# Performance work log

Measured on AMD Instinct MI355X. Metric: run time of the kernel, lower is better.

Reference implementation:

```python
import jax, jax.numpy as jnp
import numpy as np

N_ATOMS = 50000
N_EDGES = 100000
ATOM_DIM = 64
BOND_DIM = 16


def setup_inputs() -> dict:
    key = jax.random.key(0)
    k1, k2, k3, k4 = jax.random.split(key, 4)
    atom_features = jax.random.normal(k1, (N_ATOMS, ATOM_DIM), dtype=jnp.float32)
    bond_features = jax.random.normal(k2, (N_EDGES, BOND_DIM), dtype=jnp.float32)
    pair_indices = jax.random.randint(k3, (N_EDGES, 2), 0, N_ATOMS, dtype=jnp.int32)
    kernel = jax.random.normal(k4, (BOND_DIM, ATOM_DIM * ATOM_DIM), dtype=jnp.float32) * (1.0 / np.sqrt(BOND_DIM))
    bias = jnp.zeros((ATOM_DIM * ATOM_DIM,), dtype=jnp.float32)
    return {"atom_features": atom_features, "bond_features": bond_features,
            "pair_indices": pair_indices, "kernel": kernel, "bias": bias}


def reference(atom_features, bond_features, pair_indices, kernel, bias):
    n_atoms, d = atom_features.shape
    # per-edge learned linear transform: [E, bond_dim] @ [bond_dim, d*d] -> [E, d, d]
    edge_mats = (bond_features @ kernel + bias).reshape(-1, d, d)
    # gather neighbor atom features (axis 0)
    neighbors = atom_features[pair_indices[:, 1]]  # [E, d]
    # batched matvec: [E, d, d] x [E, d] -> [E, d]
    transformed = jnp.einsum('eij,ej->ei', edge_mats, neighbors)
    # scatter-add to source atoms (true segment_sum, no one-hot materialization)
    aggregated = jax.ops.segment_sum(transformed, pair_indices[:, 0], num_segments=n_atoms)
    return aggregated
```

## Files before the change

### kernel.cpp

```cpp
#include <hip/hip_runtime.h>
#include <hip/hip_bf16.h>


#define N_EDGES   100000
#define DIM       64
#define BDIM      16
#define NB_CH     17
#define KSTEPS    68
#define TILE      32
#define NTILES    (N_EDGES / TILE)
#define GROUPS    4
#define BLOCK     512
#define GRID      256

#define W_BYTES      (KSTEPS * 2 * 64 * 16)
#define NBQ_BYTES    (TILE * DIM * 2)
#define BOND_STRIDE  20
#define BOND_BYTES   (TILE * BOND_STRIDE * 2)
#define SRC_BYTES    (TILE * 4)
#define GROUP_BYTES  (NBQ_BYTES + BOND_BYTES + SRC_BYTES)
#define LDS_TOTAL    (W_BYTES + GROUPS * GROUP_BYTES)

typedef __bf16 bf16x8 __attribute__((ext_vector_type(8)));
typedef float  f32x16 __attribute__((ext_vector_type(16)));

__global__ __launch_bounds__(BLOCK, 2)
void edge_mfma_kernel(const float* __restrict__ atom,
                      const float* __restrict__ bondf,
                      const int*   __restrict__ pair,
                      const float* __restrict__ kmat,
                      const float* __restrict__ bias,
                      float* __restrict__ out)
{
    extern __shared__ char smem[];
    const int tid = threadIdx.x;

    for (int it = 0; it < (KSTEPS * 2 * 64) / BLOCK; ++it) {
        int f   = it * BLOCK + tid;
        int fb  = f >> 6;
        int l   = f & 63;
        int s   = fb >> 1, h = fb & 1;
        int kk0 = s * 16 + ((l >> 5) << 3);
        int n   = h * 32 + (l & 31);
        int b   = kk0 >> 6;
        int jj0 = kk0 & 63;
        const float* src = (b < BDIM) ? (kmat + b * (DIM * DIM) + n * DIM + jj0)
                                      : (bias + n * DIM + jj0);
        float4 v0 = *(const float4*)(src);
        float4 v1 = *(const float4*)(src + 4);
        bf16x8 w;
        w[0] = (__bf16)v0.x; w[1] = (__bf16)v0.y; w[2] = (__bf16)v0.z; w[3] = (__bf16)v0.w;
        w[4] = (__bf16)v1.x; w[5] = (__bf16)v1.y; w[6] = (__bf16)v1.z; w[7] = (__bf16)v1.w;
        *(bf16x8*)(smem + f * 16) = w;
    }
    __syncthreads();

    const int g   = tid >> 7;
    const int tg  = tid & 127;
    const int l   = tid & 63;
    const int wid = tid >> 6;
    const int h   = wid & 1;
    const int ma  = l & 31;
    const int hi  = l >> 5;

    char*   gbase = smem + W_BYTES + g * GROUP_BYTES;
    char*   nbb   = gbase;
    __bf16* bnd   = (__bf16*)(gbase + NBQ_BYTES);
    int*    srcs  = (int*)(gbase + NBQ_BYTES + BOND_BYTES);

    for (int base = blockIdx.x * GROUPS; base < NTILES; base += gridDim.x * GROUPS) {
        int  tile  = base + g;
        bool valid = tile < NTILES;

        if (valid) {
            int m = tg >> 2, p = tg & 3;
            int e = tile * TILE + m;
            int dst = pair[2 * e + 1];
            const float4* ap = (const float4*)(atom + dst * DIM + p * 16);
            float4 a0 = ap[0], a1 = ap[1], a2 = ap[2], a3 = ap[3];
            bf16x8 q0, q1;
            q0[0] = (__bf16)a0.x; q0[1] = (__bf16)a0.y; q0[2] = (__bf16)a0.z; q0[3] = (__bf16)a0.w;
            q0[4] = (__bf16)a1.x; q0[5] = (__bf16)a1.y; q0[6] = (__bf16)a1.z; q0[7] = (__bf16)a1.w;
            q1[0] = (__bf16)a2.x; q1[1] = (__bf16)a2.y; q1[2] = (__bf16)a2.z; q1[3] = (__bf16)a2.w;
            q1[4] = (__bf16)a3.x; q1[5] = (__bf16)a3.y; q1[6] = (__bf16)a3.z; q1[7] = (__bf16)a3.w;
            int sw = m & 7;
            *(bf16x8*)(nbb + m * 128 + (((2 * p    ) ^ sw) << 4)) = q0;
            *(bf16x8*)(nbb + m * 128 + (((2 * p + 1) ^ sw) << 4)) = q1;
            if (p == 0) srcs[m] = pair[2 * e];
            if (tg < TILE) {
                int m2 = tg;
                int e2 = tile * TILE + m2;
                const float4* bp = (const float4*)(bondf + e2 * BDIM);
                float4 b0 = bp[0], b1 = bp[1], b2 = bp[2], b3 = bp[3];
                __bf16* br = bnd + m2 * BOND_STRIDE;
                br[0]  = (__bf16)b0.x; br[1]  = (__bf16)b0.y; br[2]  = (__bf16)b0.z; br[3]  = (__bf16)b0.w;
                br[4]  = (__bf16)b1.x; br[5]  = (__bf16)b1.y; br[6]  = (__bf16)b1.z; br[7]  = (__bf16)b1.w;
                br[8]  = (__bf16)b2.x; br[9]  = (__bf16)b2.y; br[10] = (__bf16)b2.z; br[11] = (__bf16)b2.w;
                br[12] = (__bf16)b3.x; br[13] = (__bf16)b3.y; br[14] = (__bf16)b3.z; br[15] = (__bf16)b3.w;
                br[16] = (__bf16)1.0f;
            }
        }
        __syncthreads();

        if (valid) {
            f32x16 acc;
            #pragma unroll
            for (int i = 0; i < 16; ++i) acc[i] = 0.0f;

            const char*   nbrow = nbb + ma * 128;
            const int     sw    = ma & 7;
            const __bf16* brow  = bnd + ma * BOND_STRIDE;
            const char*   wbase = smem + (h * 64 + l) * 16;

            for (int b = 0; b < NB_CH; ++b) {
                float bv = (float)brow[b];
                #pragma unroll
                for (int ss = 0; ss < 4; ++ss) {
                    bf16x8 nv = *(const bf16x8*)(nbrow + (((ss * 2 + hi) ^ sw) << 4));
                    bf16x8 a;
                    #pragma unroll
                    for (int j = 0; j < 8; ++j)
                        a[j] = (__bf16)(bv * (float)nv[j]);
                    bf16x8 w = *(const bf16x8*)(wbase + (b * 4 + ss) * 2048);
                    acc = __builtin_amdgcn_mfma_f32_32x32x16_bf16(a, w, acc, 0, 0, 0);
                }
            }

            int n = h * 32 + (l & 31);
            #pragma unroll
            for (int r = 0; r < 16; ++r) {
                int m = (r & 3) + 8 * (r >> 2) + 4 * hi;
                atomicAdd(out + srcs[m] * DIM + n, acc[r]);
            }
        }
        __syncthreads();
    }
}

extern "C" void kernel_launch(void* const* d_in, const int* in_sizes, int n_in,
                              void* d_out, int out_size, void* d_ws, size_t ws_size,
                              hipStream_t stream)
{
    const float* atom  = (const float*)d_in[0];
    const float* bondf = (const float*)d_in[1];
    const int*   pair  = (const int*)  d_in[2];
    const float* kmat  = (const float*)d_in[3];
    const float* bias  = (const float*)d_in[4];
    float* out = (float*)d_out;

    hipFuncSetAttribute((const void*)edge_mfma_kernel,
                        hipFuncAttributeMaxDynamicSharedMemorySize, LDS_TOTAL);
    hipMemsetAsync(out, 0, (size_t)out_size * sizeof(float), stream);
    edge_mfma_kernel<<<GRID, BLOCK, LDS_TOTAL, stream>>>(atom, bondf, pair, kmat, bias, out);
}
```

Baseline: 124.0 us.

## Keep edge weights in registers, split K across waves, double-buffer tile staging

Each wave now loads its share of the bf16 weight fragments (36 k-steps) into registers once, so the weights are no longer re-read from LDS for every MFMA. The K dimension is split between two wave quartets; partial accumulators are combined through LDS before a single set of atomic adds. Gather staging is double-buffered so the next tile's neighbor and bond loads overlap with the current tile's MFMAs, and the LDS region that held the weights is reused for these buffers. The cost is much higher VGPR pressure, which limits occupancy to one block per CU, plus an extra LDS round-trip and sync to combine partial results.

```diff
diff --git a/kernel.cpp b/kernel.cpp
--- a/kernel.cpp
+++ b/kernel.cpp
@@ -5,26 +5,23 @@
 #define N_EDGES   100000
 #define DIM       64
 #define BDIM      16
-#define NB_CH     17
-#define KSTEPS    68
 #define TILE      32
 #define NTILES    (N_EDGES / TILE)
-#define GROUPS    4
 #define BLOCK     512
 #define GRID      256
+#define NKS       36
 
-#define W_BYTES      (KSTEPS * 2 * 64 * 16)
-#define NBQ_BYTES    (TILE * DIM * 2)
-#define BOND_STRIDE  20
-#define BOND_BYTES   (TILE * BOND_STRIDE * 2)
-#define SRC_BYTES    (TILE * 4)
-#define GROUP_BYTES  (NBQ_BYTES + BOND_BYTES + SRC_BYTES)
-#define LDS_TOTAL    (W_BYTES + GROUPS * GROUP_BYTES)
+#define W_BYTES      (68 * 2 * 64 * 16)
+#define NB_OFF(p,g)   (((p)*2+(g)) * 8192)
+#define BOND_OFF(p,g) (32768 + ((p)*2+(g)) * 2560)
+#define SRC_OFF(p,g)  (43008 + ((p)*2+(g)) * 128)
+#define COMB_OFF(p,g,h) (43520 + ((((p)*2+(g))*2)+(h)) * 4096)
+#define LDS_TOTAL    W_BYTES
 
 typedef __bf16 bf16x8 __attribute__((ext_vector_type(8)));
 typedef float  f32x16 __attribute__((ext_vector_type(16)));
 
-__global__ __launch_bounds__(BLOCK, 2)
+__global__ __launch_bounds__(BLOCK)
 void edge_mfma_kernel(const float* __restrict__ atom,
                       const float* __restrict__ bondf,
                       const int*   __restrict__ pair,
@@ -35,13 +32,13 @@
     extern __shared__ char smem[];
     const int tid = threadIdx.x;
 
-    for (int it = 0; it < (KSTEPS * 2 * 64) / BLOCK; ++it) {
+    for (int it = 0; it < (68 * 2 * 64) / BLOCK; ++it) {
         int f   = it * BLOCK + tid;
         int fb  = f >> 6;
-        int l   = f & 63;
-        int s   = fb >> 1, h = fb & 1;
-        int kk0 = s * 16 + ((l >> 5) << 3);
-        int n   = h * 32 + (l & 31);
+        int l_  = f & 63;
+        int s   = fb >> 1, hh = fb & 1;
+        int kk0 = s * 16 + ((l_ >> 5) << 3);
+        int n   = hh * 32 + (l_ & 31);
         int b   = kk0 >> 6;
         int jj0 = kk0 & 63;
         const float* src = (b < BDIM) ? (kmat + b * (DIM * DIM) + n * DIM + jj0)
@@ -55,85 +52,124 @@
     }
     __syncthreads();
 
-    const int g   = tid >> 7;
-    const int tg  = tid & 127;
     const int l   = tid & 63;
     const int wid = tid >> 6;
+    const int q   = wid >> 2;
+    const int g   = (wid >> 1) & 1;
     const int h   = wid & 1;
     const int ma  = l & 31;
     const int hi  = l >> 5;
 
-    char*   gbase = smem + W_BYTES + g * GROUP_BYTES;
-    char*   nbb   = gbase;
-    __bf16* bnd   = (__bf16*)(gbase + NBQ_BYTES);
-    int*    srcs  = (int*)(gbase + NBQ_BYTES + BOND_BYTES);
+    bf16x8 wfr[NKS];
+    #pragma unroll
+    for (int ks = 0; ks < NKS; ++ks) {
+        int s = q * 32 + ks;
+        wfr[ks] = *(const bf16x8*)(smem + ((s * 2 + h) * 64 + l) * 16);
+    }
+    __syncthreads();
 
-    for (int base = blockIdx.x * GROUPS; base < NTILES; base += gridDim.x * GROUPS) {
-        int  tile  = base + g;
-        bool valid = tile < NTILES;
+    const int tb0 = blockIdx.x * 2;
 
-        if (valid) {
-            int m = tg >> 2, p = tg & 3;
-            int e = tile * TILE + m;
+    auto stage = [&](int nbase, int pbuf) {
+        int sg = tid >> 8;
+        int st = tid & 255;
+        int sm = st >> 3, sp = st & 7;
+        int stile = nbase + sg;
+        if (stile < NTILES) {
+            int e   = stile * TILE + sm;
             int dst = pair[2 * e + 1];
-            const float4* ap = (const float4*)(atom + dst * DIM + p * 16);
-            float4 a0 = ap[0], a1 = ap[1], a2 = ap[2], a3 = ap[3];
-            bf16x8 q0, q1;
-            q0[0] = (__bf16)a0.x; q0[1] = (__bf16)a0.y; q0[2] = (__bf16)a0.z; q0[3] = (__bf16)a0.w;
-            q0[4] = (__bf16)a1.x; q0[5] = (__bf16)a1.y; q0[6] = (__bf16)a1.z; q0[7] = (__bf16)a1.w;
-            q1[0] = (__bf16)a2.x; q1[1] = (__bf16)a2.y; q1[2] = (__bf16)a2.z; q1[3] = (__bf16)a2.w;
-            q1[4] = (__bf16)a3.x; q1[5] = (__bf16)a3.y; q1[6] = (__bf16)a3.z; q1[7] = (__bf16)a3.w;
-            int sw = m & 7;
-            *(bf16x8*)(nbb + m * 128 + (((2 * p    ) ^ sw) << 4)) = q0;
-            *(bf16x8*)(nbb + m * 128 + (((2 * p + 1) ^ sw) << 4)) = q1;
-            if (p == 0) srcs[m] = pair[2 * e];
-            if (tg < TILE) {
-                int m2 = tg;
-                int e2 = tile * TILE + m2;
-                const float4* bp = (const float4*)(bondf + e2 * BDIM);
-                float4 b0 = bp[0], b1 = bp[1], b2 = bp[2], b3 = bp[3];
-                __bf16* br = bnd + m2 * BOND_STRIDE;
-                br[0]  = (__bf16)b0.x; br[1]  = (__bf16)b0.y; br[2]  = (__bf16)b0.z; br[3]  = (__bf16)b0.w;
-                br[4]  = (__bf16)b1.x; br[5]  = (__bf16)b1.y; br[6]  = (__bf16)b1.z; br[7]  = (__bf16)b1.w;
-                br[8]  = (__bf16)b2.x; br[9]  = (__bf16)b2.y; br[10] = (__bf16)b2.z; br[11] = (__bf16)b2.w;
-                br[12] = (__bf16)b3.x; br[13] = (__bf16)b3.y; br[14] = (__bf16)b3.z; br[15] = (__bf16)b3.w;
-                br[16] = (__bf16)1.0f;
+            const float4* ap = (const float4*)(atom + dst * DIM + sp * 8);
+            float4 v0 = ap[0], v1 = ap[1];
+            float* nbb = (float*)(smem + NB_OFF(pbuf, sg));
+            int c0 = 2 * sp, c1 = 2 * sp + 1;
+            *(float4*)(nbb + sm * 64 + ((c0 ^ (sm & 7)) << 2)) = v0;
+            *(float4*)(nbb + sm * 64 + ((c1 ^ (sm & 7)) << 2)) = v1;
+            float* bb = (float*)(smem + BOND_OFF(pbuf, sg));
+            bb[sm * 20 + sp * 2]     = bondf[e * BDIM + sp * 2];
+            bb[sm * 20 + sp * 2 + 1] = bondf[e * BDIM + sp * 2 + 1];
+            if (sp == 0) {
+                bb[sm * 20 + 16] = 1.0f;
+                ((int*)(smem + SRC_OFF(pbuf, sg)))[sm] = pair[2 * e];
             }
         }
+    };
+
+    stage(tb0, 0);
+    __syncthreads();
+
+    for (int it = 0;; ++it) {
+        const int p     = it & 1;
+        const int tile  = tb0 + it * 512 + g;
+        const int nbase = tb0 + (it + 1) * 512;
+        const bool more = (nbase < NTILES);
+        const bool valid = (tile < NTILES);
+
+        if (more) stage(nbase, p ^ 1);
+
+        f32x16 fa;
+        int oaddr[16];
+        if (valid) {
+            const float* nbb = (const float*)(smem + NB_OFF(p, g));
+            const float* bb  = (const float*)(smem + BOND_OFF(p, g));
+
+            float nbf[32];
+            #pragma unroll
+            for (int ss = 0; ss < 4; ++ss) {
+                int cb = ss * 4 + hi * 2;
+                float4 u0 = *(const float4*)(nbb + ma * 64 + (((cb)     ^ (ma & 7)) << 2));
+                float4 u1 = *(const float4*)(nbb + ma * 64 + (((cb + 1) ^ (ma & 7)) << 2));
+                nbf[ss*8+0] = u0.x; nbf[ss*8+1] = u0.y; nbf[ss*8+2] = u0.z; nbf[ss*8+3] = u0.w;
+                nbf[ss*8+4] = u1.x; nbf[ss*8+5] = u1.y; nbf[ss*8+6] = u1.z; nbf[ss*8+7] = u1.w;
+            }
+            float4 bq0 = *(const float4*)(bb + ma * 20 + q * 8);
+            float4 bq1 = *(const float4*)(bb + ma * 20 + q * 8 + 4);
+            float  b8v = bb[ma * 20 + q * 8 + 8];
+            float bnd[9] = { bq0.x, bq0.y, bq0.z, bq0.w,
+                             bq1.x, bq1.y, bq1.z, bq1.w,
+                             (q == 0) ? 0.0f : b8v };
+
+            f32x16 ac0, ac1;
+            #pragma unroll
+            for (int i = 0; i < 16; ++i) { ac0[i] = 0.0f; ac1[i] = 0.0f; }
+
+            #pragma unroll
+            for (int ks = 0; ks < NKS; ++ks) {
+                const int bi = ks >> 2, ss = ks & 3;
+                const float bv = bnd[bi];
+                bf16x8 a;
+                a[0] = (__bf16)(bv * nbf[ss*8+0]); a[1] = (__bf16)(bv * nbf[ss*8+1]);
+                a[2] = (__bf16)(bv * nbf[ss*8+2]); a[3] = (__bf16)(bv * nbf[ss*8+3]);
+                a[4] = (__bf16)(bv * nbf[ss*8+4]); a[5] = (__bf16)(bv * nbf[ss*8+5]);
+                a[6] = (__bf16)(bv * nbf[ss*8+6]); a[7] = (__bf16)(bv * nbf[ss*8+7]);
+                if (ks & 1) ac1 = __builtin_amdgcn_mfma_f32_32x32x16_bf16(a, wfr[ks], ac1, 0, 0, 0);
+                else        ac0 = __builtin_amdgcn_mfma_f32_32x32x16_bf16(a, wfr[ks], ac0, 0, 0, 0);
+            }
+            #pragma unroll
+            for (int r = 0; r < 16; ++r) fa[r] = ac0[r] + ac1[r];
+
+            if (q == 0) {
+                const int* sr = (const int*)(smem + SRC_OFF(p, g));
+                #pragma unroll
+                for (int r = 0; r < 16; ++r) {
+                    int m = (r & 3) + 8 * (r >> 2) + 4 * hi;
+                    oaddr[r] = sr[m] * DIM + h * 32 + (l & 31);
+                }
+            } else {
+                float* cbw = (float*)(smem + COMB_OFF(p, g, h));
+                #pragma unroll
+                for (int r = 0; r < 16; ++r) cbw[r * 64 + l] = fa[r];
+            }
+        }
+
         __syncthreads();
 
-        if (valid) {
-            f32x16 acc;
+        if (valid && q == 0) {
+            const float* cbr = (const float*)(smem + COMB_OFF(p, g, h));
             #pragma unroll
-            for (int i = 0; i < 16; ++i) acc[i] = 0.0f;
-
-            const char*   nbrow = nbb + ma * 128;
-            const int     sw    = ma & 7;
-            const __bf16* brow  = bnd + ma * BOND_STRIDE;
-            const char*   wbase = smem + (h * 64 + l) * 16;
-
-            for (int b = 0; b < NB_CH; ++b) {
-                float bv = (float)brow[b];
-                #pragma unroll
-                for (int ss = 0; ss < 4; ++ss) {
-                    bf16x8 nv = *(const bf16x8*)(nbrow + (((ss * 2 + hi) ^ sw) << 4));
-                    bf16x8 a;
-                    #pragma unroll
-                    for (int j = 0; j < 8; ++j)
-                        a[j] = (__bf16)(bv * (float)nv[j]);
-                    bf16x8 w = *(const bf16x8*)(wbase + (b * 4 + ss) * 2048);
-                    acc = __builtin_amdgcn_mfma_f32_32x32x16_bf16(a, w, acc, 0, 0, 0);
-                }
-            }
-
-            int n = h * 32 + (l & 31);
-            #pragma unroll
-            for (int r = 0; r < 16; ++r) {
-                int m = (r & 3) + 8 * (r >> 2) + 4 * hi;
-                atomicAdd(out + srcs[m] * DIM + n, acc[r]);
-            }
+            for (int r = 0; r < 16; ++r)
+                atomicAdd(out + oaddr[r], fa[r] + cbr[r * 64 + l]);
         }
-        __syncthreads();
+        if (!more) break;
     }
 }
 
```

Measured after the change: 208.7 us. +68.2%, slower.
